# Optimization experiments

Hardware: AMD Instinct MI355X
Metric: run time of the kernel (lower is better)

## Reference

```python
import jax, jax.numpy as jnp
import numpy as np

B, T, L, D = 2, 32, 64, 1024
H, WS, SH = 16, 8, 4
HD = D // H
EPS = 1e-6


def setup_inputs() -> dict:
    key = jax.random.key(0)
    ks = jax.random.split(key, 12)
    f = lambda i, shape, s=1.0: jax.random.normal(ks[i], shape, dtype=jnp.float32) * s
    return {
        'audio': f(0, (B, T, L, D)),
        'video': f(1, (B, T, L, D)),
        'image': f(2, (B, T, L, D)),
        'Wq': f(3, (3, D, D), 0.02), 'Wk': f(4, (3, D, D), 0.02),
        'Wv': f(5, (3, D, D), 0.02), 'Wp': f(6, (3, D, D), 0.02),
        'bq': jnp.zeros((3, D)), 'bk': jnp.zeros((3, D)),
        'bv': jnp.zeros((3, D)), 'bp': jnp.zeros((3, D)),
        'qn': jnp.ones((3, HD)), 'kn': jnp.ones((3, HD)),
        'rpb': f(7, (3, 2 * WS - 1, H), 0.02),
        'Wg1': f(8, (3 * D, 2 * D), 0.02), 'bg1': jnp.zeros((2 * D,)),
        'Wg2': f(9, (2 * D, 3), 0.02), 'bg2': jnp.zeros((3,)),
    }


def _rms(x, w):
    # OmniRMSNorm over last dim (head_dim)
    v = jnp.mean(x * x, axis=-1, keepdims=True)
    return w * (x * jax.lax.rsqrt(v + EPS))


def _wca(q_in, kv_in, Wq, bq, Wk, bk, Wv, bv, qn, kn, rpb, Wp, bp):
    """Shifted temporal-window cross attention. q_in, kv_in: [B,T,L,D]."""
    nw = T // WS
    S = WS * L  # tokens per window
    qr = jnp.roll(q_in, -SH, axis=1).reshape(B * nw, S, D)
    kr = jnp.roll(kv_in, -SH, axis=1).reshape(B * nw, S, D)
    q = (qr @ Wq + bq).reshape(B * nw, S, H, HD).transpose(0, 2, 1, 3)
    k = (kr @ Wk + bk).reshape(B * nw, S, H, HD).transpose(0, 2, 1, 3)
    v = (kr @ Wv + bv).reshape(B * nw, S, H, HD).transpose(0, 2, 1, 3)
    q = _rms(q, qn)
    k = _rms(k, kn)
    attn = jnp.einsum('bhqd,bhkd->bhqk', q, k) * (HD ** -0.5)
    # relative position bias over temporal coords within window: [H, WS, WS]
    coords = jnp.arange(WS)
    idx = coords[:, None] - coords[None, :] + WS - 1
    bias = rpb[idx].transpose(2, 0, 1)
    attn = attn.reshape(B * nw, H, WS, L, WS, L) + bias[None, :, :, None, :, None]
    attn = jax.nn.softmax(attn.reshape(B * nw, H, S, S), axis=-1)
    out = jnp.einsum('bhqk,bhkd->bhqd', attn, v)
    out = out.transpose(0, 2, 1, 3).reshape(B * nw, S, D) @ Wp + bp
    out = out.reshape(B, T, L, D)
    return jnp.roll(out, SH, axis=1)


def reference(audio, video, image, Wq, Wk, Wv, Wp, bq, bk, bv, bp,
              qn, kn, rpb, Wg1, bg1, Wg2, bg2):
    pairs = [(audio, video), (video, audio), (image, video)]
    feats = []
    for j, (qm, cm) in enumerate(pairs):
        o = _wca(qm, cm, Wq[j], bq[j], Wk[j], bk[j], Wv[j], bv[j],
                 qn[j], kn[j], rpb[j], Wp[j], bp[j])
        feats.append((qm + o).reshape(B, T * L, D))
    cat = jnp.concatenate(feats, axis=-1)                 # [B, TL, 3D]
    g = jax.nn.gelu(cat @ Wg1 + bg1, approximate=False) @ Wg2 + bg2
    gates = jax.nn.softmax(g, axis=-1)                    # [B, TL, 3]
    fused = sum(gates[..., m:m + 1] * feats[m] for m in range(3))
    return fused.reshape(B, T, L, D)
```

## Files before the change

kernel.cpp:

```cpp
#include <hip/hip_runtime.h>
#include <hip/hip_bf16.h>
#include <math.h>


typedef __bf16 bf16x8 __attribute__((ext_vector_type(8)));
typedef float f32x4 __attribute__((ext_vector_type(4)));

#define ELEM4M 4194304ull
#define ELEM1M 1048576ull

__device__ __forceinline__ float b2f(short s) {
    unsigned u = ((unsigned)(unsigned short)s) << 16;
    float f; __builtin_memcpy(&f, &u, 4); return f;
}
__device__ __forceinline__ short f2b(float f) {
    unsigned u; __builtin_memcpy(&u, &f, 4);
    u = (u + 0x7fffu + ((u >> 16) & 1u)) >> 16;
    return (short)u;
}

__global__ __launch_bounds__(256) void cast_roll_k(
    const float* __restrict__ a, const float* __restrict__ v,
    const float* __restrict__ im, short* __restrict__ dst)
{
    int z = blockIdx.y;
    const float* src = (z == 0) ? a : ((z == 1) ? v : im);
    int i = (blockIdx.x * 256 + threadIdx.x) * 4;
    int row = i >> 10, d = i & 1023;
    int b = row >> 11, tp = (row >> 6) & 31, l = row & 63;
    int srow = (b << 11) + (((tp + 4) & 31) << 6) + l;
    float4 val = *(const float4*)(src + (size_t)srow * 1024 + d);
    short4 o;
    o.x = f2b(val.x); o.y = f2b(val.y); o.z = f2b(val.z); o.w = f2b(val.w);
    *(short4*)(dst + (size_t)z * ELEM4M + i) = o;
}

__device__ __forceinline__ void transpose_body(const float* __restrict__ src,
                                               short* __restrict__ dst, int K, int N)
{
    __shared__ float tile[32][33];
    int x = blockIdx.x * 32 + threadIdx.x;
    int y0 = blockIdx.y * 32;
#pragma unroll
    for (int i = 0; i < 32; i += 8)
        tile[threadIdx.y + i][threadIdx.x] = src[(size_t)(y0 + threadIdx.y + i) * N + x];
    __syncthreads();
    int x2 = y0 + threadIdx.x;
    int y2 = blockIdx.x * 32 + threadIdx.y;
#pragma unroll
    for (int i = 0; i < 32; i += 8)
        dst[(size_t)(y2 + i) * K + x2] = f2b(tile[threadIdx.x][threadIdx.y + i]);
}

__global__ void transpose_qkvp_k(const float* Wq, const float* Wk, const float* Wv,
                                 const float* Wp, short* dst)
{
    int z = blockIdx.z;
    int g = z / 3, j = z - g * 3;
    const float* s4[4] = {Wq, Wk, Wv, Wp};
    transpose_body(s4[g] + (size_t)j * ELEM1M, dst + (size_t)z * ELEM1M, 1024, 1024);
}

__global__ void transpose_wg1_k(const float* Wg1, short* dst)
{
    transpose_body(Wg1, dst, 3072, 2048);
}

__global__ __launch_bounds__(256) void transpose_v_k(const short* __restrict__ V,
                                                     short* __restrict__ Vt)
{
    __shared__ short tile[64][65];
    int j = blockIdx.z;
    int c0 = blockIdx.x * 64, t0 = blockIdx.y * 64;
    const short* src = V + (size_t)j * ELEM4M;
    short* dst = Vt + (size_t)j * ELEM4M;
    int x = threadIdx.x & 63, y4 = threadIdx.x >> 6;
#pragma unroll
    for (int i = 0; i < 16; i++) {
        int row = y4 * 16 + i;
        tile[row][x] = src[(size_t)(t0 + row) * 1024 + c0 + x];
    }
    __syncthreads();
#pragma unroll
    for (int i = 0; i < 16; i++) {
        int row = y4 * 16 + i;
        dst[(size_t)(c0 + row) * 4096 + t0 + x] = tile[x][row];
    }
}

template<bool GELU, bool RES>
__device__ __forceinline__ void gemm_core(
    const short* __restrict__ A, const short* __restrict__ Wt,
    const float* __restrict__ bias, const short* __restrict__ Res,
    const float* __restrict__ nw, float nscale,
    short* __restrict__ C, int ldc, int colOff, int Ksz)
{
    __shared__ __align__(16) short As[128 * 64];
    __shared__ __align__(16) short Bs[128 * 64];
    const int tid = threadIdx.x;
    const int wave = tid >> 6, lane = tid & 63, quad = lane >> 4, l15 = lane & 15;
    const int wm = (wave & 1) * 64, wn = (wave >> 1) * 64;
    const int row0 = blockIdx.x * 128, col0 = blockIdx.y * 128;

    auto* As3 = (__attribute__((address_space(3))) short*)As;
    auto* Bs3 = (__attribute__((address_space(3))) short*)Bs;

    const int s_lane_r = ((wave * 64 + lane) >> 3);
    auto stage = [&](int k0) {
#pragma unroll
        for (int i = 0; i < 4; i++) {
            int s0 = i * 256 + wave * 64;
            int slot = s0 + lane;
            int r = slot >> 3, c = slot & 7;
            int gc = (c ^ (r & 7)) * 8;
            const short* ga = A + (size_t)(row0 + r) * Ksz + k0 + gc;
            const short* gb = Wt + (size_t)(col0 + r) * Ksz + k0 + gc;
            __builtin_amdgcn_global_load_lds(
                (const __attribute__((address_space(1))) void*)ga,
                (__attribute__((address_space(3))) void*)(As3 + s0 * 8), 16, 0, 0);
            __builtin_amdgcn_global_load_lds(
                (const __attribute__((address_space(1))) void*)gb,
                (__attribute__((address_space(3))) void*)(Bs3 + s0 * 8), 16, 0, 0);
        }
    };

    f32x4 acc[4][4];
#pragma unroll
    for (int i = 0; i < 4; i++)
#pragma unroll
        for (int jj = 0; jj < 4; jj++) acc[i][jj] = f32x4{0.f, 0.f, 0.f, 0.f};

    const int swz = l15 & 7;
    stage(0);
    for (int k0 = 0; k0 < Ksz; k0 += 64) {
        __syncthreads();
        bf16x8 af[4][2], bfr[4][2];
#pragma unroll
        for (int mi = 0; mi < 4; mi++)
#pragma unroll
            for (int ks = 0; ks < 2; ks++) {
                int coff = ((ks * 4 + quad) ^ swz) * 8;
                af[mi][ks]  = *(const bf16x8*)(As + (wm + mi * 16 + l15) * 64 + coff);
                bfr[mi][ks] = *(const bf16x8*)(Bs + (wn + mi * 16 + l15) * 64 + coff);
            }
        __syncthreads();
        if (k0 + 64 < Ksz) stage(k0 + 64);
#pragma unroll
        for (int ks = 0; ks < 2; ks++)
#pragma unroll
            for (int mi = 0; mi < 4; mi++)
#pragma unroll
                for (int ni = 0; ni < 4; ni++)
                    acc[mi][ni] = __builtin_amdgcn_mfma_f32_16x16x32_bf16(
                        af[mi][ks], bfr[ni][ks], acc[mi][ni], 0, 0, 0);
    }

    float bv4[4];
#pragma unroll
    for (int ni = 0; ni < 4; ni++) bv4[ni] = bias[col0 + wn + ni * 16 + l15];

    if (nw != nullptr) {
        float w4[4];
#pragma unroll
        for (int ni = 0; ni < 4; ni++) w4[ni] = nw[ni * 16 + l15];
#pragma unroll
        for (int mi = 0; mi < 4; mi++)
#pragma unroll
            for (int r = 0; r < 4; r++) {
                float v0 = acc[mi][0][r] + bv4[0];
                float v1 = acc[mi][1][r] + bv4[1];
                float v2 = acc[mi][2][r] + bv4[2];
                float v3 = acc[mi][3][r] + bv4[3];
                float ss = v0 * v0 + v1 * v1 + v2 * v2 + v3 * v3;
                ss += __shfl_xor(ss, 1); ss += __shfl_xor(ss, 2);
                ss += __shfl_xor(ss, 4); ss += __shfl_xor(ss, 8);
                float sc = rsqrtf(ss * (1.0f / 64.0f) + 1e-6f) * nscale;
                int row = row0 + wm + mi * 16 + quad * 4 + r;
                short* cp = C + (size_t)row * ldc + colOff + col0 + wn + l15;
                cp[0]  = f2b(v0 * sc * w4[0]);
                cp[16] = f2b(v1 * sc * w4[1]);
                cp[32] = f2b(v2 * sc * w4[2]);
                cp[48] = f2b(v3 * sc * w4[3]);
            }
    } else {
#pragma unroll
        for (int mi = 0; mi < 4; mi++)
#pragma unroll
            for (int ni = 0; ni < 4; ni++) {
                int col = col0 + wn + ni * 16 + l15;
#pragma unroll
                for (int r = 0; r < 4; r++) {
                    int row = row0 + wm + mi * 16 + quad * 4 + r;
                    float v = acc[mi][ni][r] + bv4[ni];
                    if (GELU) v = 0.5f * v * (1.0f + erff(v * 0.70710678118f));
                    if (RES)  v += b2f(Res[(size_t)row * 1024 + col]);
                    C[(size_t)row * ldc + colOff + col] = f2b(v);
                }
            }
    }
}

__global__ __launch_bounds__(256) void gemm_qkv_k(
    const short* r0, const short* r1, const short* r2,
    const short* Wt, const float* bq, const float* bk, const float* bv,
    const float* qn, const float* kn, short* qkv)
{
    int z = blockIdx.z;
    int g = z / 3, j = z - g * 3;
    const short* rolled[3] = {r0, r1, r2};
    const int kvmap[3] = {1, 0, 1};
    const short* A = (g == 0) ? rolled[j] : rolled[kvmap[j]];
    const float* bias = ((g == 0) ? bq : ((g == 1) ? bk : bv)) + j * 1024;
    const float* nw = (g == 0) ? (qn + j * 64) : ((g == 1) ? (kn + j * 64) : nullptr);
    float nscale = (g == 0) ? 0.125f : 1.0f;
    gemm_core<false, false>(A, Wt + (size_t)z * ELEM1M, bias, nullptr, nw, nscale,
                            qkv + (size_t)z * ELEM4M, 1024, 0, 1024);
}

__global__ __launch_bounds__(256) void gemm_out_k(
    const short* attnO, const short* Wt9, const float* bp,
    const short* r0, const short* r1, const short* r2, short* fcat)
{
    int j = blockIdx.z;
    const short* rolled[3] = {r0, r1, r2};
    gemm_core<false, true>(attnO + (size_t)j * ELEM4M, Wt9 + (size_t)j * ELEM1M,
                           bp + j * 1024, rolled[j], nullptr, 1.0f, fcat, 3072, j * 1024, 1024);
}

__global__ __launch_bounds__(256) void gemm_gate_k(
    const short* fcat, const short* Wg1t, const float* bg1, short* g1)
{
    gemm_core<true, false>(fcat, Wg1t, bg1, nullptr, nullptr, 1.0f, g1, 2048, 0, 3072);
}

__global__ __launch_bounds__(256, 2) void attn_k(
    const short* __restrict__ qkv, const short* __restrict__ Vt,
    const float* __restrict__ rpb, short* __restrict__ attnO)
{
    const int qhalf = blockIdx.x;
    const int win = blockIdx.y >> 4, h = blockIdx.y & 15;
    const int j = blockIdx.z;
    const int tid = threadIdx.x, wave = tid >> 6, lane = tid & 63;
    const int quad = lane >> 4, l15 = lane & 15;

    __shared__ __align__(16) short Ks[64 * 64];
    __shared__ __align__(16) short Vc[64 * 64];
    __shared__ __align__(16) short Ps[4][2][16 * 80];

    auto* Ks3 = (__attribute__((address_space(3))) short*)Ks;
    auto* Vc3 = (__attribute__((address_space(3))) short*)Vc;

    const int tq = qhalf * 4 + wave;
    const int qrow0 = win * 512 + tq * 64;
    const short* Qb = qkv + (size_t)j * ELEM4M + (size_t)qrow0 * 1024 + h * 64;
    const short* Kb = qkv + (size_t)(3 + j) * ELEM4M + (size_t)(win * 512) * 1024 + h * 64;
    const short* Vb = Vt + (size_t)j * ELEM4M + (size_t)(h * 64) * 4096 + win * 512;

    auto stage = [&](int ck) {
#pragma unroll
        for (int i = 0; i < 2; i++) {
            int s0 = (wave * 2 + i) * 64;
            int slot = s0 + lane;
            int r = slot >> 3, sw = ((slot & 7) ^ (r & 7)) * 8;
            const short* gk = Kb + (size_t)(ck * 64 + r) * 1024 + sw;
            const short* gv = Vb + (size_t)r * 4096 + ck * 64 + sw;
            __builtin_amdgcn_global_load_lds(
                (const __attribute__((address_space(1))) void*)gk,
                (__attribute__((address_space(3))) void*)(Ks3 + s0 * 8), 16, 0, 0);
            __builtin_amdgcn_global_load_lds(
                (const __attribute__((address_space(1))) void*)gv,
                (__attribute__((address_space(3))) void*)(Vc3 + s0 * 8), 16, 0, 0);
        }
    };

    bf16x8 qa[4][2];
#pragma unroll
    for (int qt = 0; qt < 4; qt++)
#pragma unroll
        for (int ks = 0; ks < 2; ks++)
            qa[qt][ks] = *(const bf16x8*)(Qb + (size_t)(qt * 16 + l15) * 1024
                                          + ks * 32 + quad * 8);

    f32x4 oacc[4][4];
#pragma unroll
    for (int qt = 0; qt < 4; qt++)
#pragma unroll
        for (int on = 0; on < 4; on++) oacc[qt][on] = f32x4{0.f, 0.f, 0.f, 0.f};
    float psum[4] = {0.f, 0.f, 0.f, 0.f};
    const float* rpbj = rpb + j * 240;

    stage(0);
    for (int ck = 0; ck < 8; ck++) {
        __syncthreads();
        bf16x8 kb[4][2], vb[4][2];
        const int swz = (l15 & 7);
#pragma unroll
        for (int t = 0; t < 4; t++)
#pragma unroll
            for (int ks = 0; ks < 2; ks++) {
                int row = t * 16 + l15;
                int off = row * 64 + (((ks * 4 + quad) ^ swz) * 8);
                kb[t][ks] = *(const bf16x8*)(Ks + off);
                vb[t][ks] = *(const bf16x8*)(Vc + off);
            }
        __syncthreads();
        if (ck < 7) stage(ck + 1);

        float bv = rpbj[(tq - ck + 7) * 16 + h];
#pragma unroll
        for (int qt = 0; qt < 4; qt++) {
            f32x4 sacc[4];
#pragma unroll
            for (int kn = 0; kn < 4; kn++) sacc[kn] = f32x4{0.f, 0.f, 0.f, 0.f};
#pragma unroll
            for (int ks = 0; ks < 2; ks++)
#pragma unroll
                for (int kn = 0; kn < 4; kn++)
                    sacc[kn] = __builtin_amdgcn_mfma_f32_16x16x32_bf16(
                        kb[kn][ks], qa[qt][ks], sacc[kn], 0, 0, 0);

            short* Pw = &Ps[wave][qt & 1][0];
            float ps = 0.f;
#pragma unroll
            for (int kn = 0; kn < 4; kn++) {
                float p0 = __expf(sacc[kn][0] + bv);
                float p1 = __expf(sacc[kn][1] + bv);
                float p2 = __expf(sacc[kn][2] + bv);
                float p3 = __expf(sacc[kn][3] + bv);
                ps += (p0 + p1) + (p2 + p3);
                short4 pk;
                pk.x = f2b(p0); pk.y = f2b(p1); pk.z = f2b(p2); pk.w = f2b(p3);
                *(short4*)(Pw + l15 * 80 + kn * 16 + quad * 4) = pk;
            }
            psum[qt] += ps;
#pragma unroll
            for (int ks = 0; ks < 2; ks++) {
                bf16x8 pa = *(const bf16x8*)(Pw + l15 * 80 + ks * 32 + quad * 8);
#pragma unroll
                for (int on = 0; on < 4; on++)
                    oacc[qt][on] = __builtin_amdgcn_mfma_f32_16x16x32_bf16(
                        pa, vb[on][ks], oacc[qt][on], 0, 0, 0);
            }
        }
    }

    short* Op = attnO + (size_t)j * ELEM4M;
#pragma unroll
    for (int qt = 0; qt < 4; qt++) {
        float s = psum[qt];
        s += __shfl_xor(s, 16); s += __shfl_xor(s, 32);
        float inv = 1.0f / s;
        float invr[4];
#pragma unroll
        for (int r = 0; r < 4; r++) invr[r] = __shfl(inv, quad * 4 + r);
#pragma unroll
        for (int on = 0; on < 4; on++) {
            int col = h * 64 + on * 16 + l15;
#pragma unroll
            for (int r = 0; r < 4; r++) {
                int row = qrow0 + qt * 16 + quad * 4 + r;
                Op[(size_t)row * 1024 + col] = f2b(oacc[qt][on][r] * invr[r]);
            }
        }
    }
}

__global__ __launch_bounds__(256) void fuse_k(
    const short* __restrict__ g1, const short* __restrict__ fcat,
    const float* __restrict__ Wg2, const float* __restrict__ bg2,
    float* __restrict__ out)
{
    int row = blockIdx.x, tid = threadIdx.x;
    const short* gp = g1 + (size_t)row * 2048;
    float a0 = 0.f, a1 = 0.f, a2 = 0.f;
    for (int k = tid; k < 2048; k += 256) {
        float gv = b2f(gp[k]);
        a0 += gv * Wg2[k * 3 + 0];
        a1 += gv * Wg2[k * 3 + 1];
        a2 += gv * Wg2[k * 3 + 2];
    }
#pragma unroll
    for (int off = 1; off < 64; off <<= 1) {
        a0 += __shfl_xor(a0, off); a1 += __shfl_xor(a1, off); a2 += __shfl_xor(a2, off);
    }
    __shared__ float part[4][3];
    int wave = tid >> 6, lane = tid & 63;
    if (lane == 0) { part[wave][0] = a0; part[wave][1] = a1; part[wave][2] = a2; }
    __syncthreads();
    float g0 = part[0][0] + part[1][0] + part[2][0] + part[3][0] + bg2[0];
    float gA = part[0][1] + part[1][1] + part[2][1] + part[3][1] + bg2[1];
    float gB = part[0][2] + part[1][2] + part[2][2] + part[3][2] + bg2[2];
    float mx = fmaxf(g0, fmaxf(gA, gB));
    float e0 = __expf(g0 - mx), e1 = __expf(gA - mx), e2 = __expf(gB - mx);
    float inv = 1.0f / (e0 + e1 + e2);
    e0 *= inv; e1 *= inv; e2 *= inv;

    int b = row >> 11, tp = (row >> 6) & 31, l = row & 63;
    size_t orow = (size_t)(b * 32 + ((tp + 4) & 31)) * 64 + l;
    const short* f0 = fcat + (size_t)row * 3072;
    float* op = out + orow * 1024;
    for (int c = tid; c < 1024; c += 256)
        op[c] = e0 * b2f(f0[c]) + e1 * b2f(f0[1024 + c]) + e2 * b2f(f0[2048 + c]);
}

extern "C" void kernel_launch(void* const* d_in, const int* in_sizes, int n_in,
                              void* d_out, int out_size, void* d_ws, size_t ws_size,
                              hipStream_t stream)
{
    const float* audio = (const float*)d_in[0];
    const float* video = (const float*)d_in[1];
    const float* image = (const float*)d_in[2];
    const float* Wq = (const float*)d_in[3];
    const float* Wk = (const float*)d_in[4];
    const float* Wv = (const float*)d_in[5];
    const float* Wp = (const float*)d_in[6];
    const float* bq = (const float*)d_in[7];
    const float* bk = (const float*)d_in[8];
    const float* bv = (const float*)d_in[9];
    const float* bp = (const float*)d_in[10];
    const float* qn = (const float*)d_in[11];
    const float* kn = (const float*)d_in[12];
    const float* rpb = (const float*)d_in[13];
    const float* Wg1 = (const float*)d_in[14];
    const float* bg1 = (const float*)d_in[15];
    const float* Wg2 = (const float*)d_in[16];
    const float* bg2 = (const float*)d_in[17];
    float* out = (float*)d_out;

    short* ws = (short*)d_ws;
    short* rolled = ws;
    short* Wt     = rolled + 3 * ELEM4M;
    short* Wg1t   = Wt + 12 * ELEM1M;
    short* qkv    = Wg1t + 6 * ELEM1M;
    short* attnO  = qkv + 9 * ELEM4M;
    short* fcat   = attnO + 3 * ELEM4M;
    short* VtBuf  = fcat;
    short* g1buf  = qkv;

    cast_roll_k<<<dim3(4096, 3), 256, 0, stream>>>(audio, video, image, rolled);
    transpose_qkvp_k<<<dim3(32, 32, 12), dim3(32, 8), 0, stream>>>(Wq, Wk, Wv, Wp, Wt);
    transpose_wg1_k<<<dim3(64, 96), dim3(32, 8), 0, stream>>>(Wg1, Wg1t);
    gemm_qkv_k<<<dim3(32, 8, 9), 256, 0, stream>>>(
        rolled, rolled + ELEM4M, rolled + 2 * ELEM4M, Wt, bq, bk, bv, qn, kn, qkv);
    transpose_v_k<<<dim3(16, 64, 3), 256, 0, stream>>>(qkv + 6 * ELEM4M, VtBuf);
    attn_k<<<dim3(2, 128, 3), 256, 0, stream>>>(qkv, VtBuf, rpb, attnO);
    gemm_out_k<<<dim3(32, 8, 3), 256, 0, stream>>>(
        attnO, Wt + 9 * ELEM1M, bp, rolled, rolled + ELEM4M, rolled + 2 * ELEM4M, fcat);
    gemm_gate_k<<<dim3(32, 16), 256, 0, stream>>>(fcat, Wg1t, bg1, g1buf);
    fuse_k<<<4096, 256, 0, stream>>>(g1buf, fcat, Wg2, bg2, out);
}
```

Before: 432.1 us.

## Fuse prep kernels, fold Wg2 projection into gate GEMM epilogue, raise occupancy

Merges the input cast/roll and the two weight-transpose kernels into one launch. The gate GEMM epilogue now applies GELU and projects onto Wg2 directly, accumulating the three gate logits per row with atomics. This removes the bf16 g1 intermediate write and read and leaves the fuse kernel with only softmax and blend. It also raises launch_bounds occupancy hints on the GEMM and attention kernels, which risks register spills, and adds a memset plus atomic contention and nondeterministic summation order.

After: 1.011 ms. +134.0%, slower.

```diff
diff --git a/kernel.cpp b/kernel.cpp
--- a/kernel.cpp
+++ b/kernel.cpp
@@ -19,51 +19,61 @@
     return (short)u;
 }
 
-__global__ __launch_bounds__(256) void cast_roll_k(
+__device__ __forceinline__ void transpose_body(
+    float (*tile)[33], const float* __restrict__ src, short* __restrict__ dst,
+    int K, int N, int bx, int by, int tid)
+{
+    int tx = tid & 31, ty = tid >> 5;
+    int x = bx * 32 + tx;
+    int y0 = by * 32;
+#pragma unroll
+    for (int i = 0; i < 32; i += 8)
+        tile[ty + i][tx] = src[(size_t)(y0 + ty + i) * N + x];
+    __syncthreads();
+    int x2 = y0 + tx;
+    int y2 = bx * 32 + ty;
+#pragma unroll
+    for (int i = 0; i < 32; i += 8)
+        dst[(size_t)(y2 + i) * K + x2] = f2b(tile[tx][ty + i]);
+}
+
+__global__ __launch_bounds__(256) void prep_k(
     const float* __restrict__ a, const float* __restrict__ v,
-    const float* __restrict__ im, short* __restrict__ dst)
-{
-    int z = blockIdx.y;
-    const float* src = (z == 0) ? a : ((z == 1) ? v : im);
-    int i = (blockIdx.x * 256 + threadIdx.x) * 4;
-    int row = i >> 10, d = i & 1023;
-    int b = row >> 11, tp = (row >> 6) & 31, l = row & 63;
-    int srow = (b << 11) + (((tp + 4) & 31) << 6) + l;
-    float4 val = *(const float4*)(src + (size_t)srow * 1024 + d);
-    short4 o;
-    o.x = f2b(val.x); o.y = f2b(val.y); o.z = f2b(val.z); o.w = f2b(val.w);
-    *(short4*)(dst + (size_t)z * ELEM4M + i) = o;
-}
-
-__device__ __forceinline__ void transpose_body(const float* __restrict__ src,
-                                               short* __restrict__ dst, int K, int N)
+    const float* __restrict__ im, short* __restrict__ rolled,
+    const float* __restrict__ Wq, const float* __restrict__ Wk,
+    const float* __restrict__ Wv, const float* __restrict__ Wp,
+    short* __restrict__ Wt,
+    const float* __restrict__ Wg1, short* __restrict__ Wg1t)
 {
     __shared__ float tile[32][33];
-    int x = blockIdx.x * 32 + threadIdx.x;
-    int y0 = blockIdx.y * 32;
-#pragma unroll
-    for (int i = 0; i < 32; i += 8)
-        tile[threadIdx.y + i][threadIdx.x] = src[(size_t)(y0 + threadIdx.y + i) * N + x];
-    __syncthreads();
-    int x2 = y0 + threadIdx.x;
-    int y2 = blockIdx.x * 32 + threadIdx.y;
-#pragma unroll
-    for (int i = 0; i < 32; i += 8)
-        dst[(size_t)(y2 + i) * K + x2] = f2b(tile[threadIdx.x][threadIdx.y + i]);
-}
-
-__global__ void transpose_qkvp_k(const float* Wq, const float* Wk, const float* Wv,
-                                 const float* Wp, short* dst)
-{
-    int z = blockIdx.z;
-    int g = z / 3, j = z - g * 3;
-    const float* s4[4] = {Wq, Wk, Wv, Wp};
-    transpose_body(s4[g] + (size_t)j * ELEM1M, dst + (size_t)z * ELEM1M, 1024, 1024);
-}
-
-__global__ void transpose_wg1_k(const float* Wg1, short* dst)
-{
-    transpose_body(Wg1, dst, 3072, 2048);
+    int bid = blockIdx.x, tid = threadIdx.x;
+    if (bid < 12288) {
+        int z = bid >> 12, xblk = bid & 4095;
+        const float* src = (z == 0) ? a : ((z == 1) ? v : im);
+        int i = (xblk * 256 + tid) * 4;
+        int row = i >> 10, d = i & 1023;
+        int b = row >> 11, tp = (row >> 6) & 31, l = row & 63;
+        int srow = (b << 11) + (((tp + 4) & 31) << 6) + l;
+        float4 val = *(const float4*)(src + (size_t)srow * 1024 + d);
+        short4 o;
+        o.x = f2b(val.x); o.y = f2b(val.y); o.z = f2b(val.z); o.w = f2b(val.w);
+        *(short4*)(rolled + (size_t)z * ELEM4M + i) = o;
+        return;
+    }
+    bid -= 12288;
+    if (bid < 12288) {
+        int bx = bid & 31, by = (bid >> 5) & 31, z = bid >> 10;
+        int g = z / 3, j = z - g * 3;
+        const float* s4[4] = {Wq, Wk, Wv, Wp};
+        transpose_body(tile, s4[g] + (size_t)j * ELEM1M,
+                       Wt + (size_t)z * ELEM1M, 1024, 1024, bx, by, tid);
+        return;
+    }
+    bid -= 12288;
+    {
+        int bx = bid & 63, by = bid >> 6;
+        transpose_body(tile, Wg1, Wg1t, 3072, 2048, bx, by, tid);
+    }
 }
 
 __global__ __launch_bounds__(256) void transpose_v_k(const short* __restrict__ V,
@@ -88,11 +98,12 @@
     }
 }
 
-template<bool GELU, bool RES>
+template<int MODE, bool RES>
 __device__ __forceinline__ void gemm_core(
     const short* __restrict__ A, const short* __restrict__ Wt,
     const float* __restrict__ bias, const short* __restrict__ Res,
     const float* __restrict__ nw, float nscale,
+    const float* __restrict__ Wg2, float* __restrict__ gates,
     short* __restrict__ C, int ldc, int colOff, int Ksz)
 {
     __shared__ __align__(16) short As[128 * 64];
@@ -105,7 +116,6 @@
     auto* As3 = (__attribute__((address_space(3))) short*)As;
     auto* Bs3 = (__attribute__((address_space(3))) short*)Bs;
 
-    const int s_lane_r = ((wave * 64 + lane) >> 3);
     auto stage = [&](int k0) {
 #pragma unroll
         for (int i = 0; i < 4; i++) {
@@ -159,7 +169,7 @@
 #pragma unroll
     for (int ni = 0; ni < 4; ni++) bv4[ni] = bias[col0 + wn + ni * 16 + l15];
 
-    if (nw != nullptr) {
+    if (MODE == 1) {
         float w4[4];
 #pragma unroll
         for (int ni = 0; ni < 4; ni++) w4[ni] = nw[ni * 16 + l15];
@@ -182,6 +192,41 @@
                 cp[32] = f2b(v2 * sc * w4[2]);
                 cp[48] = f2b(v3 * sc * w4[3]);
             }
+    } else if (MODE == 2) {
+        float w2[4][3];
+#pragma unroll
+        for (int ni = 0; ni < 4; ni++) {
+            int col = col0 + wn + ni * 16 + l15;
+            w2[ni][0] = Wg2[col * 3 + 0];
+            w2[ni][1] = Wg2[col * 3 + 1];
+            w2[ni][2] = Wg2[col * 3 + 2];
+        }
+#pragma unroll
+        for (int mi = 0; mi < 4; mi++)
+#pragma unroll
+            for (int r = 0; r < 4; r++) {
+                float p0 = 0.f, p1 = 0.f, p2 = 0.f;
+#pragma unroll
+                for (int ni = 0; ni < 4; ni++) {
+                    float vv = acc[mi][ni][r] + bv4[ni];
+                    vv = 0.5f * vv * (1.0f + erff(vv * 0.70710678118f));
+                    p0 += vv * w2[ni][0];
+                    p1 += vv * w2[ni][1];
+                    p2 += vv * w2[ni][2];
+                }
+#pragma unroll
+                for (int off = 1; off < 16; off <<= 1) {
+                    p0 += __shfl_xor(p0, off);
+                    p1 += __shfl_xor(p1, off);
+                    p2 += __shfl_xor(p2, off);
+                }
+                if (l15 == 0) {
+                    int row = row0 + wm + mi * 16 + quad * 4 + r;
+                    atomicAdd(&gates[row * 3 + 0], p0);
+                    atomicAdd(&gates[row * 3 + 1], p1);
+                    atomicAdd(&gates[row * 3 + 2], p2);
+                }
+            }
     } else {
 #pragma unroll
         for (int mi = 0; mi < 4; mi++)
@@ -192,15 +237,14 @@
                 for (int r = 0; r < 4; r++) {
                     int row = row0 + wm + mi * 16 + quad * 4 + r;
                     float v = acc[mi][ni][r] + bv4[ni];
-                    if (GELU) v = 0.5f * v * (1.0f + erff(v * 0.70710678118f));
-                    if (RES)  v += b2f(Res[(size_t)row * 1024 + col]);
+                    if (RES) v += b2f(Res[(size_t)row * 1024 + col]);
                     C[(size_t)row * ldc + colOff + col] = f2b(v);
                 }
             }
     }
 }
 
-__global__ __launch_bounds__(256) void gemm_qkv_k(
+__global__ __launch_bounds__(256, 4) void gemm_qkv_k(
     const short* r0, const short* r1, const short* r2,
     const short* Wt, const float* bq, const float* bk, const float* bv,
     const float* qn, const float* kn, short* qkv)
@@ -211,29 +255,37 @@
     const int kvmap[3] = {1, 0, 1};
     const short* A = (g == 0) ? rolled[j] : rolled[kvmap[j]];
     const float* bias = ((g == 0) ? bq : ((g == 1) ? bk : bv)) + j * 1024;
-    const float* nw = (g == 0) ? (qn + j * 64) : ((g == 1) ? (kn + j * 64) : nullptr);
-    float nscale = (g == 0) ? 0.125f : 1.0f;
-    gemm_core<false, false>(A, Wt + (size_t)z * ELEM1M, bias, nullptr, nw, nscale,
-                            qkv + (size_t)z * ELEM4M, 1024, 0, 1024);
-}
-
-__global__ __launch_bounds__(256) void gemm_out_k(
+    if (g == 2) {
+        gemm_core<0, false>(A, Wt + (size_t)z * ELEM1M, bias, nullptr, nullptr, 1.0f,
+                            nullptr, nullptr, qkv + (size_t)z * ELEM4M, 1024, 0, 1024);
+    } else {
+        const float* nw = (g == 0) ? (qn + j * 64) : (kn + j * 64);
+        float nscale = (g == 0) ? 0.125f : 1.0f;
+        gemm_core<1, false>(A, Wt + (size_t)z * ELEM1M, bias, nullptr, nw, nscale,
+                            nullptr, nullptr, qkv + (size_t)z * ELEM4M, 1024, 0, 1024);
+    }
+}
+
+__global__ __launch_bounds__(256, 4) void gemm_out_k(
     const short* attnO, const short* Wt9, const float* bp,
     const short* r0, const short* r1, const short* r2, short* fcat)
 {
     int j = blockIdx.z;
     const short* rolled[3] = {r0, r1, r2};
-    gemm_core<false, true>(attnO + (size_t)j * ELEM4M, Wt9 + (size_t)j * ELEM1M,
-                           bp + j * 1024, rolled[j], nullptr, 1.0f, fcat, 3072, j * 1024, 1024);
-}
-
-__global__ __launch_bounds__(256) void gemm_gate_k(
-    const short* fcat, const short* Wg1t, const float* bg1, short* g1)
-{
-    gemm_core<true, false>(fcat, Wg1t, bg1, nullptr, nullptr, 1.0f, g1, 2048, 0, 3072);
-}
-
-__global__ __launch_bounds__(256, 2) void attn_k(
+    gemm_core<0, true>(attnO + (size_t)j * ELEM4M, Wt9 + (size_t)j * ELEM1M,
+                       bp + j * 1024, rolled[j], nullptr, 1.0f, nullptr, nullptr,
+                       fcat, 3072, j * 1024, 1024);
+}
+
+__global__ __launch_bounds__(256, 4) void gemm_gate_k(
+    const short* fcat, const short* Wg1t, const float* bg1,
+    const float* Wg2, float* gates)
+{
+    gemm_core<2, false>(fcat, Wg1t, bg1, nullptr, nullptr, 1.0f, Wg2, gates,
+                        nullptr, 0, 0, 3072);
+}
+
+__global__ __launch_bounds__(256, 4) void attn_k(
     const short* __restrict__ qkv, const short* __restrict__ Vt,
     const float* __restrict__ rpb, short* __restrict__ attnO)
 {
@@ -366,30 +418,13 @@
 }
 
 __global__ __launch_bounds__(256) void fuse_k(
-    const short* __restrict__ g1, const short* __restrict__ fcat,
-    const float* __restrict__ Wg2, const float* __restrict__ bg2,
-    float* __restrict__ out)
+    const float* __restrict__ gates, const short* __restrict__ fcat,
+    const float* __restrict__ bg2, float* __restrict__ out)
 {
     int row = blockIdx.x, tid = threadIdx.x;
-    const short* gp = g1 + (size_t)row * 2048;
-    float a0 = 0.f, a1 = 0.f, a2 = 0.f;
-    for (int k = tid; k < 2048; k += 256) {
-        float gv = b2f(gp[k]);
-        a0 += gv * Wg2[k * 3 + 0];
-        a1 += gv * Wg2[k * 3 + 1];
-        a2 += gv * Wg2[k * 3 + 2];
-    }
-#pragma unroll
-    for (int off = 1; off < 64; off <<= 1) {
-        a0 += __shfl_xor(a0, off); a1 += __shfl_xor(a1, off); a2 += __shfl_xor(a2, off);
-    }
-    __shared__ float part[4][3];
-    int wave = tid >> 6, lane = tid & 63;
-    if (lane == 0) { part[wave][0] = a0; part[wave][1] = a1; part[wave][2] = a2; }
-    __syncthreads();
-    float g0 = part[0][0] + part[1][0] + part[2][0] + part[3][0] + bg2[0];
-    float gA = part[0][1] + part[1][1] + part[2][1] + part[3][1] + bg2[1];
-    float gB = part[0][2] + part[1][2] + part[2][2] + part[3][2] + bg2[2];
+    float g0 = gates[row * 3 + 0] + bg2[0];
+    float gA = gates[row * 3 + 1] + bg2[1];
+    float gB = gates[row * 3 + 2] + bg2[2];
     float mx = fmaxf(g0, fmaxf(gA, gB));
     float e0 = __expf(g0 - mx), e1 = __expf(gA - mx), e2 = __expf(gB - mx);
     float inv = 1.0f / (e0 + e1 + e2);
@@ -435,17 +470,17 @@
     short* attnO  = qkv + 9 * ELEM4M;
     short* fcat   = attnO + 3 * ELEM4M;
     short* VtBuf  = fcat;
-    short* g1buf  = qkv;
-
-    cast_roll_k<<<dim3(4096, 3), 256, 0, stream>>>(audio, video, image, rolled);
-    transpose_qkvp_k<<<dim3(32, 32, 12), dim3(32, 8), 0, stream>>>(Wq, Wk, Wv, Wp, Wt);
-    transpose_wg1_k<<<dim3(64, 96), dim3(32, 8), 0, stream>>>(Wg1, Wg1t);
+    float* gates  = (float*)qkv;
+
+    prep_k<<<30720, 256, 0, stream>>>(audio, video, image, rolled,
+                                      Wq, Wk, Wv, Wp, Wt, Wg1, Wg1t);
     gemm_qkv_k<<<dim3(32, 8, 9), 256, 0, stream>>>(
         rolled, rolled + ELEM4M, rolled + 2 * ELEM4M, Wt, bq, bk, bv, qn, kn, qkv);
     transpose_v_k<<<dim3(16, 64, 3), 256, 0, stream>>>(qkv + 6 * ELEM4M, VtBuf);
     attn_k<<<dim3(2, 128, 3), 256, 0, stream>>>(qkv, VtBuf, rpb, attnO);
+    hipMemsetAsync(gates, 0, 4096 * 3 * sizeof(float), stream);
     gemm_out_k<<<dim3(32, 8, 3), 256, 0, stream>>>(
         attnO, Wt + 9 * ELEM1M, bp, rolled, rolled + ELEM4M, rolled + 2 * ELEM4M, fcat);
-    gemm_gate_k<<<dim3(32, 16), 256, 0, stream>>>(fcat, Wg1t, bg1, g1buf);
-    fuse_k<<<4096, 256, 0, stream>>>(g1buf, fcat, Wg2, bg2, out);
-}
+    gemm_gate_k<<<dim3(32, 16), 256, 0, stream>>>(fcat, Wg1t, bg1, Wg2, gates);
+    fuse_k<<<4096, 256, 0, stream>>>(gates, fcat, bg2, out);
+}
```
